# Kernel tuning notes

Hardware: AMD Instinct MI355X
Metric: run time of the kernel (lower is better)

Reference implementation:

```python
import jax, jax.numpy as jnp
import numpy as np

N_BATCH = 128   # C: number of PWL channels / generator batch
N_PTS = 32768   # N: samples per channel
K_PWL = 20      # breakpoints per piecewise-linear function
LATENT = 8
HID = 8
EPS = 1e-7


def _mlp(z, W1, b1, W2, b2):
    # torch mlp: Linear -> Tanh -> Linear -> Tanh
    h = jnp.tanh(z @ W1 + b1)
    return jnp.tanh(h @ W2 + b2)


def _normalize01(a):
    # per-row min/max normalization, a: [C, N]
    a = a - a.min(axis=1, keepdims=True)
    return a / a.max(axis=1, keepdims=True)


def _calibrate1d(x, xp, yp):
    # x: [N, C], xp/yp: [C, K]
    N, C = x.shape
    K = xp.shape[1]
    bp = jnp.concatenate([x[:, :, None], jnp.broadcast_to(xp[None], (N, C, K))], axis=2)  # [N,C,K+1]
    order = jnp.argsort(bp, axis=2)                       # [N,C,K+1]
    sorted_bp = jnp.take_along_axis(bp, order, axis=2)
    x_idx = jnp.argmin(order, axis=2)                     # rank of x among breakpoints
    cand = x_idx - 1
    start_idx = jnp.where(x_idx == 0, 1, jnp.where(x_idx == K, K - 2, cand))
    end_idx = jnp.where(start_idx == cand, start_idx + 2, start_idx + 1)
    start_x = jnp.take_along_axis(sorted_bp, start_idx[..., None], axis=2)[..., 0]
    end_x = jnp.take_along_axis(sorted_bp, end_idx[..., None], axis=2)[..., 0]
    start_idx2 = jnp.where(x_idx == 0, 0, jnp.where(x_idx == K, K - 2, cand))
    yp_e = jnp.broadcast_to(yp[None], (N, C, K))
    start_y = jnp.take_along_axis(yp_e, start_idx2[..., None], axis=2)[..., 0]
    end_y = jnp.take_along_axis(yp_e, (start_idx2 + 1)[..., None], axis=2)[..., 0]
    return start_y + (x - start_x) * (end_y - start_y) / (end_x - start_x + EPS)


def setup_inputs() -> dict:
    key = jax.random.key(0)
    ks = jax.random.split(key, 16)
    s = 0.5
    f32 = jnp.float32
    return {
        "zf": jax.random.normal(ks[0], (N_BATCH, LATENT), f32),
        "zx": jax.random.normal(ks[1], (N_BATCH, N_PTS, LATENT), f32),
        "ze": jax.random.normal(ks[2], (N_BATCH, N_PTS, LATENT), f32),
        "Wx1": jax.random.normal(ks[3], (LATENT, HID), f32) * s,
        "bx1": jax.random.normal(ks[4], (HID,), f32) * s,
        "Wx2": jax.random.normal(ks[5], (HID, 1), f32) * s,
        "bx2": jax.random.normal(ks[6], (1,), f32) * s,
        "We1": jax.random.normal(ks[7], (LATENT, HID), f32) * s,
        "be1": jax.random.normal(ks[8], (HID,), f32) * s,
        "We2": jax.random.normal(ks[9], (HID, 1), f32) * s,
        "be2": jax.random.normal(ks[10], (1,), f32) * s,
        "Wf1": jax.random.normal(ks[11], (LATENT, HID), f32) * s,
        "bf1": jax.random.normal(ks[12], (HID,), f32) * s,
        "Wf2": jax.random.normal(ks[13], (HID, K_PWL), f32) * s,
        "bf2": jax.random.normal(ks[14], (K_PWL,), f32) * s,
        "directions": jax.random.randint(ks[15], (N_BATCH,), 0, 2) > 0,
    }


def reference(zf, zx, ze, Wx1, bx1, Wx2, bx2, We1, be1, We2, be2, Wf1, bf1, Wf2, bf2, directions):
    # gen_f: random ascending/descending monotone PWL per channel
    pts = _mlp(zf, Wf1, bf1, Wf2, bf2)                        # [C, K]
    asc = jnp.sort(pts, axis=1)
    yp = jnp.where(directions[:, None], asc, asc[:, ::-1])    # [C, K]
    xp = jnp.broadcast_to(jnp.linspace(0.0, 1.0, K_PWL, dtype=pts.dtype)[None, :], yp.shape)
    # forward_x: cause variable, per-channel normalized to [0,1]
    x = _mlp(zx, Wx1, bx1, Wx2, bx2)[..., 0]                  # [C, N]
    x = _normalize01(x).T                                     # [N, C]
    # forward_e: standardized noise (global mean / unbiased std)
    e = _mlp(ze, We1, be1, We2, be2)[..., 0].T                # [N, C]
    e = (e - e.mean()) / e.std(ddof=1)
    # forward_y
    y = _calibrate1d(x, xp, yp) + 0.1 * e                     # [N, C]
    return y
```

## Files before the change

### kernel.cpp

```cpp
#include <hip/hip_runtime.h>
#include <hip/hip_cooperative_groups.h>

namespace cg = cooperative_groups;

#define C_CH  128
#define NP    32768
#define K_PWL 20
#define LAT   8
#define HID   8
#define SLOTS 32
#define PTS   4
#define NBLK  512
#define TN    64

__device__ __forceinline__ float fast_tanh(float x) {
    float e = __expf(2.0f * x);
    return fmaf(-2.0f, __builtin_amdgcn_rcpf(e + 1.0f), 1.0f);
}

__device__ __forceinline__ unsigned fenc(float f) {
    unsigned u = __float_as_uint(f);
    return (u & 0x80000000u) ? ~u : (u | 0x80000000u);
}
__device__ __forceinline__ float fdec(unsigned e) {
    unsigned u = (e & 0x80000000u) ? (e ^ 0x80000000u) : ~e;
    return __uint_as_float(u);
}

__device__ __forceinline__ float mlp_eval(const float* W, float4 r0, float4 r1) {
    float acc = W[80];
    #pragma unroll
    for (int j = 0; j < HID; j++) {
        float hh = W[64 + j];
        hh = fmaf(r0.x, W[0 * 8 + j], hh);
        hh = fmaf(r0.y, W[1 * 8 + j], hh);
        hh = fmaf(r0.z, W[2 * 8 + j], hh);
        hh = fmaf(r0.w, W[3 * 8 + j], hh);
        hh = fmaf(r1.x, W[4 * 8 + j], hh);
        hh = fmaf(r1.y, W[5 * 8 + j], hh);
        hh = fmaf(r1.z, W[6 * 8 + j], hh);
        hh = fmaf(r1.w, W[7 * 8 + j], hh);
        acc = fmaf(fast_tanh(hh), W[72 + j], acc);
    }
    return fast_tanh(acc);
}

__global__ __launch_bounds__(256, 2)
void fused(const float* __restrict__ zf, const float* __restrict__ zx,
           const float* __restrict__ ze,
           const float* __restrict__ Wx1, const float* __restrict__ bx1,
           const float* __restrict__ Wx2, const float* __restrict__ bx2,
           const float* __restrict__ We1, const float* __restrict__ be1,
           const float* __restrict__ We2, const float* __restrict__ be2,
           const float* __restrict__ Wf1, const float* __restrict__ bf1,
           const float* __restrict__ Wf2, const float* __restrict__ bf2,
           const unsigned char* __restrict__ dirs_raw,
           float* __restrict__ out,
           double* __restrict__ psum,
           float* __restrict__ pmin,
           float* __restrict__ pmax,
           float* __restrict__ gmm,
           float* __restrict__ gstat) {
    __shared__ float sx[C_CH * (TN + 1)];
    __shared__ float se[C_CH * TN];
    __shared__ float syp[C_CH * K_PWL];
    __shared__ float sw[162];
    __shared__ float smin[C_CH], sinv[C_CH];
    __shared__ float sstat2[2];
    __shared__ float rf[8];
    __shared__ double rsd[8];
    __shared__ int is_i32;

    int t = threadIdx.x;
    int b = blockIdx.x;
    int w = t >> 6, lane = t & 63;

    if (t < 64)        sw[t] = Wx1[t];
    else if (t < 72)   sw[t] = bx1[t - 64];
    else if (t < 80)   sw[t] = Wx2[t - 72];
    else if (t == 80)  sw[80] = bx2[0];
    else if (t < 145)  sw[t] = We1[t - 81];
    else if (t < 153)  sw[t] = be1[t - 145];
    else if (t < 161)  sw[t] = We2[t - 153];
    else if (t == 161) sw[161] = be2[0];
    if (t == 192) {
        const int* di = (const int*)dirs_raw;
        int ok = 1;
        for (int i = 0; i < 32; i++) { int v = di[i]; if (v != 0 && v != 1) ok = 0; }
        is_i32 = ok;
    }
    __syncthreads();

    int n0 = b * TN;
    const float4* zx4 = (const float4*)zx + ((size_t)w * NP + n0 + lane) * 2;
    const float4* ze4 = (const float4*)ze + ((size_t)w * NP + n0 + lane) * 2;
    const size_t STEP = (size_t)4 * NP * 2;

    float ssum = 0.f, ss2 = 0.f;
    float4 A0 = zx4[0], A1 = zx4[1], AE0 = ze4[0], AE1 = ze4[1];
    float4 B0 = zx4[STEP], B1 = zx4[STEP + 1], BE0 = ze4[STEP], BE1 = ze4[STEP + 1];
    #pragma unroll 2
    for (int i = 0; i < 32; i++) {
        float4 C0, C1, CE0, CE1;
        if (i + 2 < 32) {
            size_t o = (size_t)(i + 2) * STEP;
            C0 = zx4[o]; C1 = zx4[o + 1]; CE0 = ze4[o]; CE1 = ze4[o + 1];
        } else { C0 = B0; C1 = B1; CE0 = BE0; CE1 = BE1; }
        float xv = mlp_eval(sw, A0, A1);
        float ev = mlp_eval(sw + 81, AE0, AE1);
        int idx = i * 256 + t;
        sx[idx + (idx >> 6)] = xv;
        se[idx] = ev;
        ssum += ev;
        ss2 = fmaf(ev, ev, ss2);
        A0 = B0; A1 = B1; AE0 = BE0; AE1 = BE1;
        B0 = C0; B1 = C1; BE0 = CE0; BE1 = CE1;
    }

    #pragma unroll
    for (int o = 32; o > 0; o >>= 1) {
        ssum += __shfl_down(ssum, o);
        ss2  += __shfl_down(ss2, o);
    }
    if (lane == 0) { rf[w] = ssum; rf[4 + w] = ss2; }
    __syncthreads();

    if (t < C_CH) {
        float mn = 3.0e38f, mx = -3.0e38f;
        int base = t * (TN + 1);
        #pragma unroll 8
        for (int j = 0; j < TN; j++) {
            float v = sx[base + j];
            mn = fminf(mn, v); mx = fmaxf(mx, v);
        }
        pmin[b * C_CH + t] = mn;
        pmax[b * C_CH + t] = mx;
        if (t == 0) {
            double S  = (double)rf[0] + (double)rf[1] + (double)rf[2] + (double)rf[3];
            double S2 = (double)rf[4] + (double)rf[5] + (double)rf[6] + (double)rf[7];
            psum[2 * b] = S; psum[2 * b + 1] = S2;
        }
    } else {
        int c = t - 128;
        float z[LAT];
        #pragma unroll
        for (int l = 0; l < LAT; l++) z[l] = zf[c * LAT + l];
        float h[HID];
        #pragma unroll
        for (int j = 0; j < HID; j++) {
            float a = bf1[j];
            #pragma unroll
            for (int l = 0; l < LAT; l++) a = fmaf(z[l], Wf1[l * HID + j], a);
            h[j] = fast_tanh(a);
        }
        float p[K_PWL];
        #pragma unroll
        for (int k = 0; k < K_PWL; k++) {
            float a = bf2[k];
            #pragma unroll
            for (int j = 0; j < HID; j++) a = fmaf(h[j], Wf2[j * K_PWL + k], a);
            p[k] = fast_tanh(a);
        }
        #pragma unroll
        for (int ph = 0; ph < K_PWL; ph++) {
            #pragma unroll
            for (int k = (ph & 1); k + 1 < K_PWL; k += 2) {
                float lo = fminf(p[k], p[k + 1]);
                float hi = fmaxf(p[k], p[k + 1]);
                p[k] = lo; p[k + 1] = hi;
            }
        }
        int dir = is_i32 ? (((const int*)dirs_raw)[c] != 0) : (dirs_raw[c] != 0);
        #pragma unroll
        for (int k = 0; k < K_PWL; k++)
            syp[c * K_PWL + k] = dir ? p[k] : p[K_PWL - 1 - k];
    }

    __threadfence();
    cg::grid_group grid = cg::this_grid();
    grid.sync();

    if (b < C_CH) {
        const volatile float* vmin = pmin;
        const volatile float* vmax = pmax;
        float mn = fminf(vmin[(size_t)t * C_CH + b], vmin[(size_t)(t + 256) * C_CH + b]);
        float mx = fmaxf(vmax[(size_t)t * C_CH + b], vmax[(size_t)(t + 256) * C_CH + b]);
        #pragma unroll
        for (int o = 32; o > 0; o >>= 1) {
            mn = fminf(mn, __shfl_down(mn, o));
            mx = fmaxf(mx, __shfl_down(mx, o));
        }
        if (lane == 0) { rf[w] = mn; rf[4 + w] = mx; }
        __syncthreads();
        if (t == 0) {
            mn = fminf(fminf(rf[0], rf[1]), fminf(rf[2], rf[3]));
            mx = fmaxf(fmaxf(rf[4], rf[5]), fmaxf(rf[6], rf[7]));
            gmm[b] = mn; gmm[C_CH + b] = mx;
        }
    } else if (b == C_CH) {
        const volatile double* vs = psum;
        double S  = vs[2 * t]     + vs[2 * (t + 256)];
        double S2 = vs[2 * t + 1] + vs[2 * (t + 256) + 1];
        #pragma unroll
        for (int o = 32; o > 0; o >>= 1) {
            S  += __shfl_down(S, o);
            S2 += __shfl_down(S2, o);
        }
        if (lane == 0) { rsd[w] = S; rsd[4 + w] = S2; }
        __syncthreads();
        if (t == 0) {
            S  = rsd[0] + rsd[1] + rsd[2] + rsd[3];
            S2 = rsd[4] + rsd[5] + rsd[6] + rsd[7];
            double M = (double)C_CH * NP;
            double mean = S / M;
            double var = (S2 - S * S / M) / (M - 1.0);
            gstat[0] = (float)mean;
            gstat[1] = (float)(0.1 / sqrt(var));
        }
    }
    __threadfence();
    grid.sync();

    if (t < C_CH) {
        const volatile float* g = gmm;
        float mn = g[t], mx = g[C_CH + t];
        smin[t] = mn;
        sinv[t] = __builtin_amdgcn_rcpf(mx - mn);
    }
    if (t == 0) {
        const volatile float* gs = gstat;
        sstat2[0] = gs[0]; sstat2[1] = gs[1];
    }
    __syncthreads();

    const float INV_DENOM = 1.0f / (1.0f / 19.0f + 1e-7f);
    float mean = sstat2[0], escale = sstat2[1];
    #pragma unroll 4
    for (int i = 0; i < 32; i++) {
        int idx = i * 256 + t;
        int c = idx >> 6;
        float x = sx[idx + c];
        float e = se[idx];
        float xn = (x - smin[c]) * sinv[c];
        int seg = (int)floorf(xn * 19.0f);
        seg = max(0, min(18, seg));
        float y0 = syp[c * K_PWL + seg];
        float y1 = syp[c * K_PWL + seg + 1];
        float y = fmaf((xn - (float)seg * (1.0f / 19.0f)) * INV_DENOM, y1 - y0, y0);
        y = fmaf(e - mean, escale, y);
        sx[idx + c] = y;
    }
    __syncthreads();
    #pragma unroll 4
    for (int ii = 0; ii < 32; ii++) {
        int idx2 = ii * 256 + t;
        int c = idx2 & 127;
        int j = idx2 >> 7;
        out[(size_t)(n0 + j) * C_CH + c] = sx[c * (TN + 1) + j];
    }
}

__global__ void prep(const float* __restrict__ zf,
                     const float* __restrict__ Wf1, const float* __restrict__ bf1,
                     const float* __restrict__ Wf2, const float* __restrict__ bf2,
                     const unsigned char* __restrict__ dirs_raw,
                     float* __restrict__ ypw,
                     unsigned* cminE, unsigned* cmaxE, double* sums) {
    int t = threadIdx.x;
    if (t < C_CH) { cminE[t] = 0xFFFFFFFFu; cmaxE[t] = 0u; }
    if (t < 2 * SLOTS) sums[t] = 0.0;

    __shared__ int is_i32;
    if (t == 0) {
        const int* di = (const int*)dirs_raw;
        int ok = 1;
        for (int i = 0; i < 32; i++) { int v = di[i]; if (v != 0 && v != 1) ok = 0; }
        is_i32 = ok;
    }
    __syncthreads();
    if (t >= C_CH) return;
    int c = t;

    float z[LAT];
    #pragma unroll
    for (int l = 0; l < LAT; l++) z[l] = zf[c * LAT + l];
    float h[HID];
    #pragma unroll
    for (int j = 0; j < HID; j++) {
        float a = bf1[j];
        #pragma unroll
        for (int l = 0; l < LAT; l++) a = fmaf(z[l], Wf1[l * HID + j], a);
        h[j] = fast_tanh(a);
    }
    float p[K_PWL];
    #pragma unroll
    for (int k = 0; k < K_PWL; k++) {
        float a = bf2[k];
        #pragma unroll
        for (int j = 0; j < HID; j++) a = fmaf(h[j], Wf2[j * K_PWL + k], a);
        p[k] = fast_tanh(a);
    }
    for (int i = 1; i < K_PWL; i++) {
        float key = p[i];
        int j = i - 1;
        while (j >= 0 && p[j] > key) { p[j + 1] = p[j]; j--; }
        p[j + 1] = key;
    }
    int dir = is_i32 ? (((const int*)dirs_raw)[c] != 0) : (dirs_raw[c] != 0);
    for (int k = 0; k < K_PWL; k++)
        ypw[c * K_PWL + k] = dir ? p[k] : p[K_PWL - 1 - k];
}

__global__ __launch_bounds__(256)
void pass1(const float* __restrict__ zx, const float* __restrict__ ze,
           const float* __restrict__ Wx1, const float* __restrict__ bx1,
           const float* __restrict__ Wx2, const float* __restrict__ bx2,
           const float* __restrict__ We1, const float* __restrict__ be1,
           const float* __restrict__ We2, const float* __restrict__ be2,
           float* __restrict__ xraw, float* __restrict__ eraw,
           unsigned* __restrict__ cminE, unsigned* __restrict__ cmaxE,
           double* __restrict__ sums) {
    __shared__ float sw[162];
    int t = threadIdx.x;
    if (t < 64)       sw[t] = Wx1[t];
    else if (t < 72)  sw[t] = bx1[t - 64];
    else if (t < 80)  sw[t] = Wx2[t - 72];
    else if (t == 80) sw[80] = bx2[0];
    else if (t < 145) sw[t] = We1[t - 81];
    else if (t < 153) sw[t] = be1[t - 145];
    else if (t < 161) sw[t] = We2[t - 153];
    else if (t == 161) sw[161] = be2[0];
    __syncthreads();

    int c = blockIdx.y;
    int n0 = blockIdx.x * (256 * PTS) + t;
    size_t row = (size_t)c * NP;
    const float4* zx4 = (const float4*)(zx + row * LAT);
    const float4* ze4 = (const float4*)(ze + row * LAT);

    float4 ax[PTS][2], ae[PTS][2];
    #pragma unroll
    for (int k = 0; k < PTS; k++) {
        int n = n0 + k * 256;
        ax[k][0] = zx4[2 * n];  ax[k][1] = zx4[2 * n + 1];
        ae[k][0] = ze4[2 * n];  ae[k][1] = ze4[2 * n + 1];
    }

    float xv[PTS], ev[PTS];
    #pragma unroll
    for (int k = 0; k < PTS; k++) xv[k] = mlp_eval(sw, ax[k][0], ax[k][1]);
    #pragma unroll
    for (int k = 0; k < PTS; k++) ev[k] = mlp_eval(sw + 81, ae[k][0], ae[k][1]);

    float mn = xv[0], mx = xv[0], s = 0.f, s2 = 0.f;
    #pragma unroll
    for (int k = 0; k < PTS; k++) {
        xraw[row + n0 + k * 256] = xv[k];
        eraw[row + n0 + k * 256] = ev[k];
        mn = fminf(mn, xv[k]); mx = fmaxf(mx, xv[k]);
        s += ev[k]; s2 += ev[k] * ev[k];
    }

    #pragma unroll
    for (int o = 32; o > 0; o >>= 1) {
        mn = fminf(mn, __shfl_down(mn, o));
        mx = fmaxf(mx, __shfl_down(mx, o));
        s += __shfl_down(s, o);
        s2 += __shfl_down(s2, o);
    }
    __shared__ float rmn[4], rmx[4], rs[4], rs2[4];
    int wave = t >> 6, lane = t & 63;
    if (lane == 0) { rmn[wave] = mn; rmx[wave] = mx; rs[wave] = s; rs2[wave] = s2; }
    __syncthreads();
    if (t == 0) {
        for (int w = 1; w < 4; w++) {
            mn = fminf(mn, rmn[w]); mx = fmaxf(mx, rmx[w]);
            s += rs[w]; s2 += rs2[w];
        }
        atomicMin(&cminE[c], fenc(mn));
        atomicMax(&cmaxE[c], fenc(mx));
        int slot = (blockIdx.x + blockIdx.y) & (SLOTS - 1);
        atomicAdd(&sums[2 * slot], (double)s);
        atomicAdd(&sums[2 * slot + 1], (double)s2);
    }
}

__global__ __launch_bounds__(256)
void pass2(const float* __restrict__ xraw, const float* __restrict__ eraw,
           const float* __restrict__ ypw,
           const unsigned* __restrict__ cminE, const unsigned* __restrict__ cmaxE,
           const double* __restrict__ sums,
           float* __restrict__ out) {
    __shared__ float ytile[C_CH * 33];
    __shared__ float syp[C_CH * K_PWL];
    __shared__ float smin[C_CH], sinv[C_CH];
    __shared__ float sstat[2];

    int t = threadIdx.x;
    for (int i = t; i < C_CH * K_PWL; i += 256) syp[i] = ypw[i];
    if (t < C_CH) {
        float mn = fdec(cminE[t]);
        float mx = fdec(cmaxE[t]);
        smin[t] = mn;
        sinv[t] = __builtin_amdgcn_rcpf(mx - mn);
    }
    if (t == 0) {
        double s = 0.0, s2 = 0.0;
        for (int i = 0; i < SLOTS; i++) { s += sums[2 * i]; s2 += sums[2 * i + 1]; }
        double M = (double)C_CH * NP;
        double mean = s / M;
        double var = (s2 - s * s / M) / (M - 1.0);
        sstat[0] = (float)mean;
        sstat[1] = (float)(0.1 / sqrt(var));
    }
    __syncthreads();

    const float INV_DENOM = 1.0f / (1.0f / 19.0f + 1e-7f);
    float mean = sstat[0], escale = sstat[1];
    int n0 = blockIdx.x * 32;

    #pragma unroll
    for (int i = 0; i < 16; i++) {
        int idx = i * 256 + t;
        int c = idx >> 5;
        int j = idx & 31;
        size_t g = (size_t)c * NP + (n0 + j);
        float x = xraw[g];
        float e = eraw[g];
        float xn = (x - smin[c]) * sinv[c];
        int seg = (int)floorf(xn * 19.0f);
        seg = max(0, min(18, seg));
        float y0 = syp[c * K_PWL + seg];
        float y1 = syp[c * K_PWL + seg + 1];
        float y = fmaf((xn - (float)seg * (1.0f / 19.0f)) * INV_DENOM, y1 - y0, y0);
        y = fmaf(e - mean, escale, y);
        ytile[c * 33 + j] = y;
    }
    __syncthreads();
    #pragma unroll
    for (int i = 0; i < 16; i++) {
        int idx = i * 256 + t;
        int j = idx >> 7;
        int c = idx & 127;
        out[(size_t)(n0 + j) * C_CH + c] = ytile[c * 33 + j];
    }
}

extern "C" void kernel_launch(void* const* d_in, const int* in_sizes, int n_in,
                              void* d_out, int out_size, void* d_ws, size_t ws_size,
                              hipStream_t stream) {
    const float* zf  = (const float*)d_in[0];
    const float* zx  = (const float*)d_in[1];
    const float* ze  = (const float*)d_in[2];
    const float* Wx1 = (const float*)d_in[3];
    const float* bx1 = (const float*)d_in[4];
    const float* Wx2 = (const float*)d_in[5];
    const float* bx2 = (const float*)d_in[6];
    const float* We1 = (const float*)d_in[7];
    const float* be1 = (const float*)d_in[8];
    const float* We2 = (const float*)d_in[9];
    const float* be2 = (const float*)d_in[10];
    const float* Wf1 = (const float*)d_in[11];
    const float* bf1 = (const float*)d_in[12];
    const float* Wf2 = (const float*)d_in[13];
    const float* bf2 = (const float*)d_in[14];
    const unsigned char* dirs = (const unsigned char*)d_in[15];
    float* outp = (float*)d_out;

    static int mode = -1;
    if (mode < 0) {
        int dev = 0, coop = 0, nb = 0;
        hipGetDevice(&dev);
        hipDeviceGetAttribute(&coop, hipDeviceAttributeCooperativeLaunch, dev);
        hipError_t oe = hipOccupancyMaxActiveBlocksPerMultiprocessor(
            &nb, reinterpret_cast<const void*>(fused), 256, 0);
        mode = (coop && oe == hipSuccess && nb >= 2) ? 1 : 0;
    }

    if (mode == 1) {
        double* psum  = (double*)d_ws;
        float*  pmin  = (float*)(psum + 2 * NBLK);
        float*  pmax  = pmin + NBLK * C_CH;
        float*  gmm   = pmax + NBLK * C_CH;
        float*  gstat = gmm + 2 * C_CH;
        void* args[] = {
            (void*)&zf,  (void*)&zx,  (void*)&ze,
            (void*)&Wx1, (void*)&bx1, (void*)&Wx2, (void*)&bx2,
            (void*)&We1, (void*)&be1, (void*)&We2, (void*)&be2,
            (void*)&Wf1, (void*)&bf1, (void*)&Wf2, (void*)&bf2,
            (void*)&dirs, (void*)&outp,
            (void*)&psum, (void*)&pmin, (void*)&pmax, (void*)&gmm, (void*)&gstat
        };
        hipError_t le = hipLaunchCooperativeKernel(
            reinterpret_cast<const void*>(fused), dim3(NBLK), dim3(256),
            args, 0, stream);
        if (le == hipSuccess) return;
        mode = 0;
    }

    float* xraw = (float*)d_ws;
    float* eraw = xraw + (size_t)C_CH * NP;
    float* ypw  = eraw + (size_t)C_CH * NP;
    unsigned* cminE = (unsigned*)(ypw + C_CH * K_PWL);
    unsigned* cmaxE = cminE + C_CH;
    double* sums = (double*)(cmaxE + C_CH);

    hipLaunchKernelGGL(prep, dim3(1), dim3(256), 0, stream,
                       zf, Wf1, bf1, Wf2, bf2, dirs, ypw, cminE, cmaxE, sums);
    hipLaunchKernelGGL(pass1, dim3(NP / (256 * PTS), C_CH), dim3(256), 0, stream,
                       zx, ze, Wx1, bx1, Wx2, bx2, We1, be1, We2, be2,
                       xraw, eraw, cminE, cmaxE, sums);
    hipLaunchKernelGGL(pass2, dim3(NP / 32), dim3(256), 0, stream,
                       xraw, eraw, ypw, cminE, cmaxE, sums, outp);
}
```

Measured before the change: 342.0 us.

## Restructure fused kernel to per-channel chunks with global tile scratch and higher occupancy

Blocks now process contiguous point ranges of a single channel, computing min/max and noise sums directly in registers. x and e values are spilled to a global tiled scratch buffer and re-read after the grid syncs for calibration, with an XOR-swizzled shared tile and float4 transposed output. Shared memory drops so four blocks per CU and up to 1024 cooperative blocks can run. In exchange it adds extra global writes and reads of the intermediate x/e arrays.

```diff
diff --git a/kernel.cpp b/kernel.cpp
--- a/kernel.cpp
+++ b/kernel.cpp
@@ -10,8 +10,6 @@
 #define HID   8
 #define SLOTS 32
 #define PTS   4
-#define NBLK  512
-#define TN    64
 
 __device__ __forceinline__ float fast_tanh(float x) {
     float e = __expf(2.0f * x);
@@ -45,35 +43,38 @@
     return fast_tanh(acc);
 }
 
-__global__ __launch_bounds__(256, 2)
-void fused(const float* __restrict__ zf, const float* __restrict__ zx,
-           const float* __restrict__ ze,
-           const float* __restrict__ Wx1, const float* __restrict__ bx1,
-           const float* __restrict__ Wx2, const float* __restrict__ bx2,
-           const float* __restrict__ We1, const float* __restrict__ be1,
-           const float* __restrict__ We2, const float* __restrict__ be2,
-           const float* __restrict__ Wf1, const float* __restrict__ bf1,
-           const float* __restrict__ Wf2, const float* __restrict__ bf2,
-           const unsigned char* __restrict__ dirs_raw,
-           float* __restrict__ out,
-           double* __restrict__ psum,
-           float* __restrict__ pmin,
-           float* __restrict__ pmax,
-           float* __restrict__ gmm,
-           float* __restrict__ gstat) {
-    __shared__ float sx[C_CH * (TN + 1)];
-    __shared__ float se[C_CH * TN];
+__global__ __launch_bounds__(256, 4)
+void fused2(const float* __restrict__ zf, const float* __restrict__ zx,
+            const float* __restrict__ ze,
+            const float* __restrict__ Wx1, const float* __restrict__ bx1,
+            const float* __restrict__ Wx2, const float* __restrict__ bx2,
+            const float* __restrict__ We1, const float* __restrict__ be1,
+            const float* __restrict__ We2, const float* __restrict__ be2,
+            const float* __restrict__ Wf1, const float* __restrict__ bf1,
+            const float* __restrict__ Wf2, const float* __restrict__ bf2,
+            const unsigned char* __restrict__ dirs_raw,
+            float* __restrict__ out,
+            float* __restrict__ xtile,
+            float* __restrict__ etile,
+            double* __restrict__ psum,
+            float* __restrict__ pminB,
+            float* __restrict__ pmaxB,
+            float* __restrict__ gmm,
+            float* __restrict__ gstat,
+            int chLog, int nblk) {
+    __shared__ float sw[162];
+    __shared__ float rf[16];
+    __shared__ double rsd[8];
+    __shared__ float ytile[C_CH * 32];
     __shared__ float syp[C_CH * K_PWL];
-    __shared__ float sw[162];
     __shared__ float smin[C_CH], sinv[C_CH];
     __shared__ float sstat2[2];
-    __shared__ float rf[8];
-    __shared__ double rsd[8];
     __shared__ int is_i32;
 
     int t = threadIdx.x;
     int b = blockIdx.x;
     int w = t >> 6, lane = t & 63;
+    cg::grid_group grid = cg::this_grid();
 
     if (t < 64)        sw[t] = Wx1[t];
     else if (t < 72)   sw[t] = bx1[t - 64];
@@ -83,124 +84,76 @@
     else if (t < 153)  sw[t] = be1[t - 145];
     else if (t < 161)  sw[t] = We2[t - 153];
     else if (t == 161) sw[161] = be2[0];
-    if (t == 192) {
-        const int* di = (const int*)dirs_raw;
-        int ok = 1;
-        for (int i = 0; i < 32; i++) { int v = di[i]; if (v != 0 && v != 1) ok = 0; }
-        is_i32 = ok;
-    }
-    __syncthreads();
-
-    int n0 = b * TN;
-    const float4* zx4 = (const float4*)zx + ((size_t)w * NP + n0 + lane) * 2;
-    const float4* ze4 = (const float4*)ze + ((size_t)w * NP + n0 + lane) * 2;
-    const size_t STEP = (size_t)4 * NP * 2;
-
-    float ssum = 0.f, ss2 = 0.f;
-    float4 A0 = zx4[0], A1 = zx4[1], AE0 = ze4[0], AE1 = ze4[1];
-    float4 B0 = zx4[STEP], B1 = zx4[STEP + 1], BE0 = ze4[STEP], BE1 = ze4[STEP + 1];
-    #pragma unroll 2
-    for (int i = 0; i < 32; i++) {
-        float4 C0, C1, CE0, CE1;
-        if (i + 2 < 32) {
-            size_t o = (size_t)(i + 2) * STEP;
-            C0 = zx4[o]; C1 = zx4[o + 1]; CE0 = ze4[o]; CE1 = ze4[o + 1];
-        } else { C0 = B0; C1 = B1; CE0 = BE0; CE1 = BE1; }
-        float xv = mlp_eval(sw, A0, A1);
-        float ev = mlp_eval(sw + 81, AE0, AE1);
-        int idx = i * 256 + t;
-        sx[idx + (idx >> 6)] = xv;
-        se[idx] = ev;
-        ssum += ev;
-        ss2 = fmaf(ev, ev, ss2);
-        A0 = B0; A1 = B1; AE0 = BE0; AE1 = BE1;
-        B0 = C0; B1 = C1; BE0 = CE0; BE1 = CE1;
-    }
-
+    __syncthreads();
+
+    int chPer = 1 << chLog;
+    int c = b >> chLog;
+    int q = b & (chPer - 1);
+    int ppb = NP >> chLog;
+    int nbase = q * ppb;
+    int G = ppb >> 10;
+    size_t rowz = (size_t)c * NP;
+    const float4* zx4 = (const float4*)zx;
+    const float4* ze4 = (const float4*)ze;
+    int cbase = c * 32;
+
+    float mn = 3.0e38f, mx = -3.0e38f, s = 0.f, s2 = 0.f;
+    for (int g = 0; g < G; ++g) {
+        int nb0 = nbase + (g << 10) + t;
+        float4 ax[PTS][2], ae[PTS][2];
+        #pragma unroll
+        for (int k = 0; k < PTS; ++k) {
+            size_t zi = (rowz + nb0 + (k << 8)) * 2;
+            ax[k][0] = zx4[zi]; ax[k][1] = zx4[zi + 1];
+            ae[k][0] = ze4[zi]; ae[k][1] = ze4[zi + 1];
+        }
+        #pragma unroll
+        for (int k = 0; k < PTS; ++k) {
+            float xv = mlp_eval(sw, ax[k][0], ax[k][1]);
+            float ev = mlp_eval(sw + 81, ae[k][0], ae[k][1]);
+            int n = nb0 + (k << 8);
+            int addr = (n >> 5) * (C_CH * 32) + cbase + (n & 31);
+            xtile[addr] = xv;
+            etile[addr] = ev;
+            mn = fminf(mn, xv); mx = fmaxf(mx, xv);
+            s += ev; s2 = fmaf(ev, ev, s2);
+        }
+    }
     #pragma unroll
     for (int o = 32; o > 0; o >>= 1) {
-        ssum += __shfl_down(ssum, o);
-        ss2  += __shfl_down(ss2, o);
-    }
-    if (lane == 0) { rf[w] = ssum; rf[4 + w] = ss2; }
-    __syncthreads();
-
-    if (t < C_CH) {
-        float mn = 3.0e38f, mx = -3.0e38f;
-        int base = t * (TN + 1);
-        #pragma unroll 8
-        for (int j = 0; j < TN; j++) {
-            float v = sx[base + j];
-            mn = fminf(mn, v); mx = fmaxf(mx, v);
-        }
-        pmin[b * C_CH + t] = mn;
-        pmax[b * C_CH + t] = mx;
-        if (t == 0) {
-            double S  = (double)rf[0] + (double)rf[1] + (double)rf[2] + (double)rf[3];
-            double S2 = (double)rf[4] + (double)rf[5] + (double)rf[6] + (double)rf[7];
-            psum[2 * b] = S; psum[2 * b + 1] = S2;
-        }
-    } else {
-        int c = t - 128;
-        float z[LAT];
-        #pragma unroll
-        for (int l = 0; l < LAT; l++) z[l] = zf[c * LAT + l];
-        float h[HID];
-        #pragma unroll
-        for (int j = 0; j < HID; j++) {
-            float a = bf1[j];
-            #pragma unroll
-            for (int l = 0; l < LAT; l++) a = fmaf(z[l], Wf1[l * HID + j], a);
-            h[j] = fast_tanh(a);
-        }
-        float p[K_PWL];
-        #pragma unroll
-        for (int k = 0; k < K_PWL; k++) {
-            float a = bf2[k];
-            #pragma unroll
-            for (int j = 0; j < HID; j++) a = fmaf(h[j], Wf2[j * K_PWL + k], a);
-            p[k] = fast_tanh(a);
-        }
-        #pragma unroll
-        for (int ph = 0; ph < K_PWL; ph++) {
-            #pragma unroll
-            for (int k = (ph & 1); k + 1 < K_PWL; k += 2) {
-                float lo = fminf(p[k], p[k + 1]);
-                float hi = fmaxf(p[k], p[k + 1]);
-                p[k] = lo; p[k + 1] = hi;
+        mn = fminf(mn, __shfl_down(mn, o));
+        mx = fmaxf(mx, __shfl_down(mx, o));
+        s += __shfl_down(s, o);
+        s2 += __shfl_down(s2, o);
+    }
+    if (lane == 0) { rf[w] = mn; rf[4 + w] = mx; rf[8 + w] = s; rf[12 + w] = s2; }
+    __syncthreads();
+    if (t == 0) {
+        mn = fminf(fminf(rf[0], rf[1]), fminf(rf[2], rf[3]));
+        mx = fmaxf(fmaxf(rf[4], rf[5]), fmaxf(rf[6], rf[7]));
+        pminB[b] = mn; pmaxB[b] = mx;
+        psum[2 * b]     = (double)rf[8]  + (double)rf[9]  + (double)rf[10] + (double)rf[11];
+        psum[2 * b + 1] = (double)rf[12] + (double)rf[13] + (double)rf[14] + (double)rf[15];
+    }
+    __threadfence();
+    grid.sync();
+
+    if (b == 0) {
+        if (t < C_CH) {
+            const volatile float* vmin = pminB;
+            const volatile float* vmax = pmaxB;
+            float m1 = 3.0e38f, m2 = -3.0e38f;
+            for (int qq = 0; qq < chPer; ++qq) {
+                m1 = fminf(m1, vmin[(t << chLog) + qq]);
+                m2 = fmaxf(m2, vmax[(t << chLog) + qq]);
             }
-        }
-        int dir = is_i32 ? (((const int*)dirs_raw)[c] != 0) : (dirs_raw[c] != 0);
-        #pragma unroll
-        for (int k = 0; k < K_PWL; k++)
-            syp[c * K_PWL + k] = dir ? p[k] : p[K_PWL - 1 - k];
-    }
-
-    __threadfence();
-    cg::grid_group grid = cg::this_grid();
-    grid.sync();
-
-    if (b < C_CH) {
-        const volatile float* vmin = pmin;
-        const volatile float* vmax = pmax;
-        float mn = fminf(vmin[(size_t)t * C_CH + b], vmin[(size_t)(t + 256) * C_CH + b]);
-        float mx = fmaxf(vmax[(size_t)t * C_CH + b], vmax[(size_t)(t + 256) * C_CH + b]);
-        #pragma unroll
-        for (int o = 32; o > 0; o >>= 1) {
-            mn = fminf(mn, __shfl_down(mn, o));
-            mx = fmaxf(mx, __shfl_down(mx, o));
-        }
-        if (lane == 0) { rf[w] = mn; rf[4 + w] = mx; }
-        __syncthreads();
-        if (t == 0) {
-            mn = fminf(fminf(rf[0], rf[1]), fminf(rf[2], rf[3]));
-            mx = fmaxf(fmaxf(rf[4], rf[5]), fmaxf(rf[6], rf[7]));
-            gmm[b] = mn; gmm[C_CH + b] = mx;
-        }
-    } else if (b == C_CH) {
+            gmm[t] = m1; gmm[C_CH + t] = m2;
+        }
         const volatile double* vs = psum;
-        double S  = vs[2 * t]     + vs[2 * (t + 256)];
-        double S2 = vs[2 * t + 1] + vs[2 * (t + 256) + 1];
+        double S = 0.0, S2 = 0.0;
+        for (int i = t; i < nblk; i += 256) {
+            S += vs[2 * i]; S2 += vs[2 * i + 1];
+        }
         #pragma unroll
         for (int o = 32; o > 0; o >>= 1) {
             S  += __shfl_down(S, o);
@@ -217,46 +170,122 @@
             gstat[0] = (float)mean;
             gstat[1] = (float)(0.1 / sqrt(var));
         }
-    }
-    __threadfence();
+        __threadfence();
+    }
     grid.sync();
 
+    if (t == 0) {
+        const int* di = (const int*)dirs_raw;
+        int ok = 1;
+        for (int i = 0; i < 32; i++) { int v = di[i]; if (v != 0 && v != 1) ok = 0; }
+        is_i32 = ok;
+        const volatile float* gs = gstat;
+        sstat2[0] = gs[0]; sstat2[1] = gs[1];
+    }
     if (t < C_CH) {
         const volatile float* g = gmm;
-        float mn = g[t], mx = g[C_CH + t];
-        smin[t] = mn;
-        sinv[t] = __builtin_amdgcn_rcpf(mx - mn);
-    }
-    if (t == 0) {
-        const volatile float* gs = gstat;
-        sstat2[0] = gs[0]; sstat2[1] = gs[1];
+        float m1 = g[t], m2 = g[C_CH + t];
+        smin[t] = m1;
+        sinv[t] = __builtin_amdgcn_rcpf(m2 - m1);
+    }
+    __syncthreads();
+    if (t >= C_CH) {
+        int cc = t - C_CH;
+        float z[LAT];
+        #pragma unroll
+        for (int l = 0; l < LAT; l++) z[l] = zf[cc * LAT + l];
+        float h[HID];
+        #pragma unroll
+        for (int j = 0; j < HID; j++) {
+            float a = bf1[j];
+            #pragma unroll
+            for (int l = 0; l < LAT; l++) a = fmaf(z[l], Wf1[l * HID + j], a);
+            h[j] = fast_tanh(a);
+        }
+        float p[K_PWL];
+        #pragma unroll
+        for (int k = 0; k < K_PWL; k++) {
+            float a = bf2[k];
+            #pragma unroll
+            for (int j = 0; j < HID; j++) a = fmaf(h[j], Wf2[j * K_PWL + k], a);
+            p[k] = fast_tanh(a);
+        }
+        #pragma unroll
+        for (int ph = 0; ph < K_PWL; ph++) {
+            #pragma unroll
+            for (int k = (ph & 1); k + 1 < K_PWL; k += 2) {
+                float lo = fminf(p[k], p[k + 1]);
+                float hi = fmaxf(p[k], p[k + 1]);
+                p[k] = lo; p[k + 1] = hi;
+            }
+        }
+        int dir = is_i32 ? (((const int*)dirs_raw)[cc] != 0) : (dirs_raw[cc] != 0);
+        #pragma unroll
+        for (int k = 0; k < K_PWL; k++)
+            syp[cc * K_PWL + k] = dir ? p[k] : p[K_PWL - 1 - k];
     }
     __syncthreads();
 
     const float INV_DENOM = 1.0f / (1.0f / 19.0f + 1e-7f);
     float mean = sstat2[0], escale = sstat2[1];
-    #pragma unroll 4
-    for (int i = 0; i < 32; i++) {
-        int idx = i * 256 + t;
-        int c = idx >> 6;
-        float x = sx[idx + c];
-        float e = se[idx];
-        float xn = (x - smin[c]) * sinv[c];
-        int seg = (int)floorf(xn * 19.0f);
-        seg = max(0, min(18, seg));
-        float y0 = syp[c * K_PWL + seg];
-        float y1 = syp[c * K_PWL + seg + 1];
-        float y = fmaf((xn - (float)seg * (1.0f / 19.0f)) * INV_DENOM, y1 - y0, y0);
-        y = fmaf(e - mean, escale, y);
-        sx[idx + c] = y;
-    }
-    __syncthreads();
-    #pragma unroll 4
-    for (int ii = 0; ii < 32; ii++) {
-        int idx2 = ii * 256 + t;
-        int c = idx2 & 127;
-        int j = idx2 >> 7;
-        out[(size_t)(n0 + j) * C_CH + c] = sx[c * (TN + 1) + j];
+    int tpb = (NP / 32) / nblk;
+
+    for (int T = b * tpb; T < b * tpb + tpb; ++T) {
+        const float4* xt4 = (const float4*)(xtile + (size_t)T * (C_CH * 32));
+        const float4* et4 = (const float4*)(etile + (size_t)T * (C_CH * 32));
+        #pragma unroll
+        for (int i = 0; i < 4; ++i) {
+            int fi = i * 256 + t;
+            float4 xv = xt4[fi];
+            float4 ev = et4[fi];
+            int cc = fi >> 3;
+            int j0 = (fi & 7) * 4;
+            float sm = smin[cc], si = sinv[cc];
+            int sb = cc * K_PWL;
+            int cb = cc * 32, cx = cc & 31;
+            {
+                float xn = (xv.x - sm) * si;
+                int seg = (int)floorf(xn * 19.0f); seg = max(0, min(18, seg));
+                float y0 = syp[sb + seg], y1 = syp[sb + seg + 1];
+                float y = fmaf((xn - (float)seg * (1.0f / 19.0f)) * INV_DENOM, y1 - y0, y0);
+                ytile[cb + ((j0 + 0) ^ cx)] = fmaf(ev.x - mean, escale, y);
+            }
+            {
+                float xn = (xv.y - sm) * si;
+                int seg = (int)floorf(xn * 19.0f); seg = max(0, min(18, seg));
+                float y0 = syp[sb + seg], y1 = syp[sb + seg + 1];
+                float y = fmaf((xn - (float)seg * (1.0f / 19.0f)) * INV_DENOM, y1 - y0, y0);
+                ytile[cb + ((j0 + 1) ^ cx)] = fmaf(ev.y - mean, escale, y);
+            }
+            {
+                float xn = (xv.z - sm) * si;
+                int seg = (int)floorf(xn * 19.0f); seg = max(0, min(18, seg));
+                float y0 = syp[sb + seg], y1 = syp[sb + seg + 1];
+                float y = fmaf((xn - (float)seg * (1.0f / 19.0f)) * INV_DENOM, y1 - y0, y0);
+                ytile[cb + ((j0 + 2) ^ cx)] = fmaf(ev.z - mean, escale, y);
+            }
+            {
+                float xn = (xv.w - sm) * si;
+                int seg = (int)floorf(xn * 19.0f); seg = max(0, min(18, seg));
+                float y0 = syp[sb + seg], y1 = syp[sb + seg + 1];
+                float y = fmaf((xn - (float)seg * (1.0f / 19.0f)) * INV_DENOM, y1 - y0, y0);
+                ytile[cb + ((j0 + 3) ^ cx)] = fmaf(ev.w - mean, escale, y);
+            }
+        }
+        __syncthreads();
+        #pragma unroll
+        for (int i = 0; i < 4; ++i) {
+            int fi = i * 256 + t;
+            int j = fi >> 5;
+            int c4 = (fi & 31) * 4;
+            float4 o;
+            o.x = ytile[(c4 + 0) * 32 + (j ^ ((c4 + 0) & 31))];
+            o.y = ytile[(c4 + 1) * 32 + (j ^ ((c4 + 1) & 31))];
+            o.z = ytile[(c4 + 2) * 32 + (j ^ ((c4 + 2) & 31))];
+            o.w = ytile[(c4 + 3) * 32 + (j ^ ((c4 + 3) & 31))];
+            ((float4*)out)[(((size_t)(T * 32 + j)) * C_CH + c4) >> 2] = o;
+        }
+        if (T + 1 < b * tpb + tpb) __syncthreads();
     }
 }
 
@@ -469,30 +498,43 @@
 
     static int mode = -1;
     if (mode < 0) {
-        int dev = 0, coop = 0, nb = 0;
+        int dev = 0, coop = 0, nb = 0, mpc = 0;
         hipGetDevice(&dev);
         hipDeviceGetAttribute(&coop, hipDeviceAttributeCooperativeLaunch, dev);
+        hipDeviceGetAttribute(&mpc, hipDeviceAttributeMultiprocessorCount, dev);
         hipError_t oe = hipOccupancyMaxActiveBlocksPerMultiprocessor(
-            &nb, reinterpret_cast<const void*>(fused), 256, 0);
-        mode = (coop && oe == hipSuccess && nb >= 2) ? 1 : 0;
-    }
-
-    if (mode == 1) {
-        double* psum  = (double*)d_ws;
-        float*  pmin  = (float*)(psum + 2 * NBLK);
-        float*  pmax  = pmin + NBLK * C_CH;
-        float*  gmm   = pmax + NBLK * C_CH;
-        float*  gstat = gmm + 2 * C_CH;
+            &nb, reinterpret_cast<const void*>(fused2), 256, 0);
+        mode = 0;
+        if (coop && oe == hipSuccess && mpc > 0) {
+            long cap = (long)nb * mpc;
+            if (cap >= 1024) mode = 2;
+            else if (cap >= 512) mode = 1;
+        }
+    }
+
+    size_t need = (size_t)2 * C_CH * NP * 4 + 2 * 1024 * 8 + (2 * 1024 + 256 + 2) * 4;
+    if (mode >= 1 && ws_size >= need) {
+        float*  xtile = (float*)d_ws;
+        float*  etile = xtile + (size_t)C_CH * NP;
+        double* psum  = (double*)(etile + (size_t)C_CH * NP);
+        float*  pminB = (float*)(psum + 2 * 1024);
+        float*  pmaxB = pminB + 1024;
+        float*  gmm   = pmaxB + 1024;
+        float*  gstat = gmm + 256;
+        int nblk  = (mode == 2) ? 1024 : 512;
+        int chLog = (mode == 2) ? 3 : 2;
         void* args[] = {
             (void*)&zf,  (void*)&zx,  (void*)&ze,
             (void*)&Wx1, (void*)&bx1, (void*)&Wx2, (void*)&bx2,
             (void*)&We1, (void*)&be1, (void*)&We2, (void*)&be2,
             (void*)&Wf1, (void*)&bf1, (void*)&Wf2, (void*)&bf2,
             (void*)&dirs, (void*)&outp,
-            (void*)&psum, (void*)&pmin, (void*)&pmax, (void*)&gmm, (void*)&gstat
+            (void*)&xtile, (void*)&etile, (void*)&psum,
+            (void*)&pminB, (void*)&pmaxB, (void*)&gmm, (void*)&gstat,
+            (void*)&chLog, (void*)&nblk
         };
         hipError_t le = hipLaunchCooperativeKernel(
-            reinterpret_cast<const void*>(fused), dim3(NBLK), dim3(256),
+            reinterpret_cast<const void*>(fused2), dim3(nblk), dim3(256),
             args, 0, stream);
         if (le == hipSuccess) return;
         mode = 0;
```

New measurement: 837.9 us. 2.45x slower.
